# Kernel tuning notes

Measured on AMD Instinct MI355X. Metric: run time of the kernel, lower is better.

## Reference

```python
import jax, jax.numpy as jnp
import numpy as np

NX = 768
N_HEAD = 12
N_CTX = 2048
BATCH = 4
EPS = 1e-5
NEG = -1000000000.0


def _layernorm(x, g, b):
    # NOTE: faithful to source bug: returns g + normalized + b (additive, not scale)
    u = jnp.mean(x, axis=-1, keepdims=True)
    s = jnp.mean((x - u) ** 2, axis=-1, keepdims=True)
    return g + (x - u) / jnp.sqrt(s + EPS) + b


def setup_inputs() -> dict:
    key = jax.random.key(0)
    ks = jax.random.split(key, 8)
    std = 0.02
    x = jax.random.normal(ks[0], (BATCH, N_CTX, NX), dtype=jnp.float32)
    w_attn = jax.random.normal(ks[1], (NX, 3 * NX), dtype=jnp.float32) * std
    b_attn = jnp.zeros((3 * NX,), jnp.float32)
    w_proj = jax.random.normal(ks[2], (NX, NX), dtype=jnp.float32) * std
    b_proj = jnp.zeros((NX,), jnp.float32)
    ln1_g = jnp.ones((NX,), jnp.float32)
    ln1_b = jnp.zeros((NX,), jnp.float32)
    w_fc = jax.random.normal(ks[3], (NX, 4 * NX), dtype=jnp.float32) * std
    b_fc = jnp.zeros((4 * NX,), jnp.float32)
    w_fc2 = jax.random.normal(ks[4], (4 * NX, NX), dtype=jnp.float32) * std
    b_fc2 = jnp.zeros((NX,), jnp.float32)
    ln2_g = jnp.ones((NX,), jnp.float32)
    ln2_b = jnp.zeros((NX,), jnp.float32)
    return dict(x=x, w_attn=w_attn, b_attn=b_attn, w_proj=w_proj, b_proj=b_proj,
                ln1_g=ln1_g, ln1_b=ln1_b, w_fc=w_fc, b_fc=b_fc,
                w_fc2=w_fc2, b_fc2=b_fc2, ln2_g=ln2_g, ln2_b=ln2_b)


def reference(x, w_attn, b_attn, w_proj, b_proj, ln1_g, ln1_b,
              w_fc, b_fc, w_fc2, b_fc2, ln2_g, ln2_b):
    B, S, D = x.shape
    dh = D // N_HEAD
    # --- attention (scale=False: no 1/sqrt(d)) ---
    qkv = x @ w_attn + b_attn                      # [B,S,3D]
    q, k, v = jnp.split(qkv, 3, axis=-1)
    q = q.reshape(B, S, N_HEAD, dh).transpose(0, 2, 1, 3)   # [B,H,S,dh]
    k = k.reshape(B, S, N_HEAD, dh).transpose(0, 2, 3, 1)   # [B,H,dh,S]
    v = v.reshape(B, S, N_HEAD, dh).transpose(0, 2, 1, 3)   # [B,H,S,dh]
    w = jnp.einsum('bhsd,bhdt->bhst', q, k)        # [B,H,S,S]
    mask = jnp.tril(jnp.ones((S, S), x.dtype))[None, None]
    w = w * mask + NEG * (1.0 - mask)
    w = jax.nn.softmax(w, axis=-1)
    a = jnp.einsum('bhst,bhtd->bhsd', w, v)        # [B,H,S,dh]
    a = a.transpose(0, 2, 1, 3).reshape(B, S, D)
    a = a @ w_proj + b_proj
    # dropout layers are identity (eval mode)
    n = _layernorm(x + a, ln1_g, ln1_b)
    # --- MLP (intended ReLU; source's nn.ReLU usage is a bug) ---
    h = jax.nn.relu(n @ w_fc + b_fc)
    m = h @ w_fc2 + b_fc2
    return _layernorm(n + m, ln2_g, ln2_b)
```

## Files before the change

### kernel.cpp

```cpp
#include <hip/hip_runtime.h>
#include <stdint.h>

#define NX 768
#define SEQ 2048
#define NHEAD 12
#define MROWS 8192
#define LN_EPS 1e-5f
#define MASK_NEG -1000000000.0f

typedef __bf16 bf16x8 __attribute__((ext_vector_type(8)));
typedef float f32x4 __attribute__((ext_vector_type(4)));

#define AS3(p)  ((__attribute__((address_space(3))) void*)(p))
#define AS1C(p) ((const __attribute__((address_space(1))) void*)(p))

__device__ __forceinline__ unsigned short f2bf(float f) {
  union { float f; unsigned int u; } v; v.f = f;
  unsigned int r = v.u + 0x7fffu + ((v.u >> 16) & 1u);
  return (unsigned short)(r >> 16);
}
__device__ __forceinline__ unsigned int f2bf_fast_u(float f) {
  union { float f; unsigned int u; } v; v.f = f;
  return (v.u + 0x8000u) >> 16;
}
__device__ __forceinline__ float bf2f(unsigned short u) {
  union { unsigned int u; float f; } v; v.u = ((unsigned int)u) << 16;
  return v.f;
}

__global__ void convert_f32_bf16(const float* __restrict__ in,
                                 unsigned short* __restrict__ out, int n4) {
  int i = blockIdx.x * blockDim.x + threadIdx.x;
  if (i >= n4) return;
  float4 v = ((const float4*)in)[i];
  ushort4 o;
  o.x = f2bf(v.x); o.y = f2bf(v.y); o.z = f2bf(v.z); o.w = f2bf(v.w);
  ((ushort4*)out)[i] = o;
}

__global__ void transpose_w(const float* __restrict__ w,
                            unsigned short* __restrict__ wt, int K, int N) {
  __shared__ float tile[32][33];
  int n0 = blockIdx.x * 32, k0 = blockIdx.y * 32;
  int tx = threadIdx.x, ty = threadIdx.y;
#pragma unroll
  for (int j = 0; j < 4; ++j)
    tile[ty + j * 8][tx] = w[(long)(k0 + ty + j * 8) * N + n0 + tx];
  __syncthreads();
#pragma unroll
  for (int j = 0; j < 4; ++j)
    wt[(long)(n0 + ty + j * 8) * K + k0 + tx] = f2bf(tile[tx][ty + j * 8]);
}

__global__ void transpose_v(const unsigned short* __restrict__ qkv,
                            unsigned short* __restrict__ vt) {
  __shared__ unsigned short tile[64][68];
  int s0 = blockIdx.x * 64;
  int bh = blockIdx.y, b = bh / NHEAD, h = bh % NHEAD;
  int tx = threadIdx.x, ty = threadIdx.y;
  const unsigned short* src = qkv + (long)b * SEQ * 2304 + 1536 + h * 64;
#pragma unroll
  for (int j = 0; j < 4; ++j) {
    int s = ty + j * 16;
    ushort4 vv = *(const ushort4*)(src + (long)(s0 + s) * 2304 + tx * 4);
    *(ushort4*)(&tile[s][tx * 4]) = vv;
  }
  __syncthreads();
  unsigned short* dst = vt + (long)bh * 64 * SEQ + s0;
#pragma unroll
  for (int j = 0; j < 4; ++j) {
    int d = ty + j * 16;
    ushort4 o;
    o.x = tile[tx * 4 + 0][d]; o.y = tile[tx * 4 + 1][d];
    o.z = tile[tx * 4 + 2][d]; o.w = tile[tx * 4 + 3][d];
    *(ushort4*)(dst + (long)d * SEQ + tx * 4) = o;
  }
}

template <int ACT, int BN>
__global__ __launch_bounds__(256) void gemm_bt(const unsigned short* __restrict__ A,
                                               const unsigned short* __restrict__ Bt,
                                               const float* __restrict__ bias,
                                               unsigned short* __restrict__ C,
                                               int Nsz, int K) {
  constexpr int ABUF = 128 * 64;
  constexpr int BBUF = BN * 64;
  constexpr int BUF = ABUF + BBUF;
  __shared__ __align__(16) unsigned short smem[2 * BUF];
  const int tid = threadIdx.x;
  const int w = tid >> 6, lane = tid & 63;
  const int l15 = lane & 15, quad = lane >> 4;
  constexpr int MT = (BN == 128) ? 4 : 2;
  const int wrow0 = (BN == 128) ? (w >> 1) * 64 : w * 32;
  const int wcol0 = (BN == 128) ? (w & 1) * 64 : 0;
  const long m0 = (long)blockIdx.x * 128;
  const long n0 = (long)blockIdx.y * BN;

  const int srow = tid >> 3;
  const int sg = tid & 7;

  const unsigned short* ap[4];
#pragma unroll
  for (int p = 0; p < 4; ++p) {
    int row = p * 32 + srow;
    ap[p] = A + (m0 + row) * (long)K + (sg ^ (row & 7)) * 8;
  }
  const unsigned short* bp[BN / 32];
#pragma unroll
  for (int p = 0; p < BN / 32; ++p) {
    int row = p * 32 + srow;
    bp[p] = Bt + (n0 + row) * (long)K + (sg ^ (row & 7)) * 8;
  }

  auto stage = [&](int kb) {
    unsigned short* As = smem + (kb & 1) * BUF;
    unsigned short* Bs = As + ABUF;
#pragma unroll
    for (int p = 0; p < 4; ++p) {
      __builtin_amdgcn_global_load_lds(AS1C(ap[p]), AS3(As + p * 2048 + w * 512), 16, 0, 0);
      ap[p] += 64;
    }
#pragma unroll
    for (int p = 0; p < BN / 32; ++p) {
      __builtin_amdgcn_global_load_lds(AS1C(bp[p]), AS3(Bs + p * 2048 + w * 512), 16, 0, 0);
      bp[p] += 64;
    }
  };

  f32x4 acc[MT][4] = {};
  const int nkb = K / 64;

  stage(0);
  for (int kb = 0; kb < nkb; ++kb) {
    __syncthreads();
    if (kb + 1 < nkb) stage(kb + 1);
    const unsigned short* As = smem + (kb & 1) * BUF;
    const unsigned short* Bs = As + ABUF;
#pragma unroll
    for (int s2 = 0; s2 < 2; ++s2) {
      const int phys = ((s2 * 4 + quad) ^ (l15 & 7)) * 8;
      bf16x8 af[MT], bfr[4];
#pragma unroll
      for (int mt = 0; mt < MT; ++mt)
        af[mt] = *(const bf16x8*)(As + (wrow0 + mt * 16 + l15) * 64 + phys);
#pragma unroll
      for (int nt = 0; nt < 4; ++nt)
        bfr[nt] = *(const bf16x8*)(Bs + (wcol0 + nt * 16 + l15) * 64 + phys);
#pragma unroll
      for (int mt = 0; mt < MT; ++mt)
#pragma unroll
        for (int nt = 0; nt < 4; ++nt)
          acc[mt][nt] = __builtin_amdgcn_mfma_f32_16x16x32_bf16(af[mt], bfr[nt], acc[mt][nt], 0, 0, 0);
    }
  }
  __syncthreads();

  unsigned short* Ew = smem + w * (16 * 72);
  const long gmB = m0 + wrow0;
  const long gnB = n0 + wcol0;
  float bv[4];
#pragma unroll
  for (int nt = 0; nt < 4; ++nt) bv[nt] = bias[gnB + nt * 16 + l15];
  const int prow = lane >> 3, pcol = (lane & 7) * 8;
#pragma unroll
  for (int mt = 0; mt < MT; ++mt) {
#pragma unroll
    for (int nt = 0; nt < 4; ++nt)
#pragma unroll
      for (int r = 0; r < 4; ++r) {
        float v = acc[mt][nt][r] + bv[nt];
        if (ACT == 1) v = fmaxf(v, 0.f);
        Ew[(quad * 4 + r) * 72 + nt * 16 + l15] = f2bf(v);
      }
#pragma unroll
    for (int ps = 0; ps < 2; ++ps) {
      int row = ps * 8 + prow;
      int4 t = *(const int4*)(Ew + row * 72 + pcol);
      *(int4*)(C + (gmB + mt * 16 + row) * (long)Nsz + gnB + pcol) = t;
    }
  }
}

__global__ __launch_bounds__(256) void attn_v7(const unsigned short* __restrict__ qkv,
                                               const unsigned short* __restrict__ vt,
                                               unsigned short* __restrict__ out) {
  const int blk = blockIdx.x;
  const int bh_lo = blk & 7;
  const int j = blk >> 3;
  const int bx = j & 15;
  const int bh = (j >> 4) * 8 + bh_lo;
  const int b = bh / NHEAD, h = bh % NHEAD;
  const int tid = threadIdx.x;
  const int w = tid >> 6, lane = tid & 63, l15 = lane & 15, quad = lane >> 4;

  __shared__ __align__(16) unsigned short Ks[2][64 * 64];
  __shared__ __align__(16) unsigned short Vs[2][64 * 64];
  __shared__ __align__(16) unsigned short Ps[4][16 * 64];

  const long rowbase = (long)b * SEQ;
  unsigned short* Pw = &Ps[w][0];
  const unsigned short* vbh = vt + (long)bh * 64 * SEQ;
  const float LOG2E = 1.4426950408889634f;

  const int krow = tid >> 3;
  const int kgo = (((tid & 7) ^ (krow & 7)) * 8);
  const unsigned short* kbase = qkv + rowbase * 2304L + 768 + h * 64;

  for (int pass = 0; pass < 2; ++pass) {
    const int qt = (pass == 0) ? bx : 31 - bx;
    const int niter = qt + 1;
    const int qrow = qt * 64 + w * 16 + l15;
    const int qg = qrow;

    bf16x8 qf[2];
#pragma unroll
    for (int s2 = 0; s2 < 2; ++s2) {
      int4 raw = *(const int4*)(qkv + (rowbase + qrow) * 2304L + h * 64 + s2 * 32 + quad * 8);
      const unsigned short* rp = (const unsigned short*)&raw;
#pragma unroll
      for (int j2 = 0; j2 < 8; ++j2)
        qf[s2][j2] = (__bf16)(bf2f(rp[j2]) * LOG2E);
    }

    const unsigned short* kp[2];
    const unsigned short* vp[2];
#pragma unroll
    for (int p = 0; p < 2; ++p) {
      kp[p] = kbase + (long)(p * 32 + krow) * 2304 + kgo;
      vp[p] = vbh + (long)(p * 32 + krow) * SEQ + kgo;
    }

    float l_sum = 0.f;
    f32x4 o_acc[4] = {};

    __syncthreads();
#pragma unroll
    for (int p = 0; p < 2; ++p) {
      __builtin_amdgcn_global_load_lds(AS1C(kp[p]), AS3(&Ks[0][0] + p * 2048 + w * 512), 16, 0, 0);
      __builtin_amdgcn_global_load_lds(AS1C(vp[p]), AS3(&Vs[0][0] + p * 2048 + w * 512), 16, 0, 0);
      kp[p] += 64 * 2304;
      vp[p] += 64;
    }

    for (int it = 0; it < niter; ++it) {
      __syncthreads();
      if (it + 1 < niter) {
        const int nb = (it + 1) & 1;
#pragma unroll
        for (int p = 0; p < 2; ++p) {
          __builtin_amdgcn_global_load_lds(AS1C(kp[p]), AS3(&Ks[nb][0] + p * 2048 + w * 512), 16, 0, 0);
          __builtin_amdgcn_global_load_lds(AS1C(vp[p]), AS3(&Vs[nb][0] + p * 2048 + w * 512), 16, 0, 0);
          kp[p] += 64 * 2304;
          vp[p] += 64;
        }
      }
      const unsigned short* Kc = &Ks[it & 1][0];
      const unsigned short* Vc = &Vs[it & 1][0];

      f32x4 st[4] = {};
#pragma unroll
      for (int nt = 0; nt < 4; ++nt) {
        int key = nt * 16 + l15;
#pragma unroll
        for (int s2 = 0; s2 < 2; ++s2) {
          int phys = (s2 * 4 + quad) ^ (key & 7);
          bf16x8 kf = *(const bf16x8*)(Kc + key * 64 + phys * 8);
          st[nt] = __builtin_amdgcn_mfma_f32_16x16x32_bf16(kf, qf[s2], st[nt], 0, 0, 0);
        }
      }

      if (it == niter - 1) {
#pragma unroll
        for (int nt = 0; nt < 4; ++nt) {
          int kg = it * 64 + nt * 16 + quad * 4;
#pragma unroll
          for (int r = 0; r < 4; ++r)
            if (kg + r > qg) st[nt][r] = MASK_NEG;
        }
      }

      float psum = 0.f;
#pragma unroll
      for (int nt = 0; nt < 4; ++nt)
#pragma unroll
        for (int r = 0; r < 4; ++r) {
          float p = __builtin_amdgcn_exp2f(st[nt][r]);
          st[nt][r] = p;
          psum += p;
        }
      psum += __shfl_xor(psum, 16);
      psum += __shfl_xor(psum, 32);
      l_sum += psum;

#pragma unroll
      for (int nt = 0; nt < 4; ++nt) {
        unsigned int lo = f2bf_fast_u(st[nt][0]) | (f2bf_fast_u(st[nt][1]) << 16);
        unsigned int hi = f2bf_fast_u(st[nt][2]) | (f2bf_fast_u(st[nt][3]) << 16);
        int g8 = (nt * 2 + (quad >> 1)) ^ (l15 & 7);
        uint2 pv; pv.x = lo; pv.y = hi;
        *(uint2*)(Pw + l15 * 64 + g8 * 8 + (quad & 1) * 4) = pv;
      }

#pragma unroll
      for (int c = 0; c < 2; ++c) {
        int phys = ((c * 4 + quad) ^ (l15 & 7)) * 8;
        bf16x8 pf = *(const bf16x8*)(Pw + l15 * 64 + phys);
#pragma unroll
        for (int ntd = 0; ntd < 4; ++ntd) {
          int d = ntd * 16 + l15;
          bf16x8 vf = *(const bf16x8*)(Vc + d * 64 + phys);
          o_acc[ntd] = __builtin_amdgcn_mfma_f32_16x16x32_bf16(pf, vf, o_acc[ntd], 0, 0, 0);
        }
      }
    }

#pragma unroll
    for (int r = 0; r < 4; ++r) {
      float lq = __shfl(l_sum, quad * 4 + r);
      float inv = 1.f / lq;
      int q = qt * 64 + w * 16 + quad * 4 + r;
#pragma unroll
      for (int ntd = 0; ntd < 4; ++ntd) {
        int d = ntd * 16 + l15;
        out[(rowbase + q) * (long)NX + h * 64 + d] = f2bf(o_acc[ntd][r] * inv);
      }
    }
  }
}

__global__ __launch_bounds__(256) void add_ln(const float* __restrict__ x_f,
                                              const unsigned short* __restrict__ x_b,
                                              const unsigned short* __restrict__ y_b,
                                              const float* __restrict__ g,
                                              const float* __restrict__ beta,
                                              float* __restrict__ out_f,
                                              unsigned short* __restrict__ out_b) {
  const int row = blockIdx.x, t = threadIdx.x;
  const long base = (long)row * NX;
  float v[3];
#pragma unroll
  for (int j = 0; j < 3; ++j) {
    int i = t + j * 256;
    float a = x_f ? x_f[base + i] : bf2f(x_b[base + i]);
    v[j] = a + bf2f(y_b[base + i]);
  }
  __shared__ float red[4];
  int wv = t >> 6, ln = t & 63;

  float ssum = v[0] + v[1] + v[2];
#pragma unroll
  for (int sh = 32; sh >= 1; sh >>= 1) ssum += __shfl_xor(ssum, sh);
  if (ln == 0) red[wv] = ssum;
  __syncthreads();
  float u = (red[0] + red[1] + red[2] + red[3]) * (1.f / NX);
  __syncthreads();

  float d0 = v[0] - u, d1 = v[1] - u, d2 = v[2] - u;
  float sq = d0 * d0 + d1 * d1 + d2 * d2;
#pragma unroll
  for (int sh = 32; sh >= 1; sh >>= 1) sq += __shfl_xor(sq, sh);
  if (ln == 0) red[wv] = sq;
  __syncthreads();
  float s = (red[0] + red[1] + red[2] + red[3]) * (1.f / NX);
  float rinv = rsqrtf(s + LN_EPS);

  float dd[3] = {d0, d1, d2};
#pragma unroll
  for (int j = 0; j < 3; ++j) {
    int i = t + j * 256;
    float o = g[i] + dd[j] * rinv + beta[i];
    if (out_f) out_f[base + i] = o;
    else out_b[base + i] = f2bf(o);
  }
}

extern "C" void kernel_launch(void* const* d_in, const int* in_sizes, int n_in,
                              void* d_out, int out_size, void* d_ws, size_t ws_size,
                              hipStream_t stream) {
  const float* x      = (const float*)d_in[0];
  const float* w_attn = (const float*)d_in[1];
  const float* b_attn = (const float*)d_in[2];
  const float* w_proj = (const float*)d_in[3];
  const float* b_proj = (const float*)d_in[4];
  const float* ln1_g  = (const float*)d_in[5];
  const float* ln1_b  = (const float*)d_in[6];
  const float* w_fc   = (const float*)d_in[7];
  const float* b_fc   = (const float*)d_in[8];
  const float* w_fc2  = (const float*)d_in[9];
  const float* b_fc2  = (const float*)d_in[10];
  const float* ln2_g  = (const float*)d_in[11];
  const float* ln2_b  = (const float*)d_in[12];
  float* out = (float*)d_out;

  char* ws = (char*)d_ws;
  size_t off = 0;
  auto alloc = [&](size_t bytes) {
    char* p = ws + off;
    off += (bytes + 255) & ~(size_t)255;
    return p;
  };
  unsigned short* xb      = (unsigned short*)alloc((size_t)MROWS * NX * 2);
  unsigned short* wt_attn = (unsigned short*)alloc((size_t)2304 * 768 * 2);
  unsigned short* wt_proj = (unsigned short*)alloc((size_t)768 * 768 * 2);
  unsigned short* wt_fc   = (unsigned short*)alloc((size_t)3072 * 768 * 2);
  unsigned short* wt_fc2  = (unsigned short*)alloc((size_t)768 * 3072 * 2);
  unsigned short* qkv     = (unsigned short*)alloc((size_t)MROWS * 3072 * 2);
  unsigned short* hbuf    = qkv;
  unsigned short* abuf    = (unsigned short*)alloc((size_t)MROWS * NX * 2);
  unsigned short* mbuf    = abuf;
  unsigned short* nbuf    = (unsigned short*)alloc((size_t)MROWS * NX * 2);
  unsigned short* vtb     = nbuf;
  unsigned short* pout    = xb;

  convert_f32_bf16<<<(MROWS * NX / 4 + 255) / 256, 256, 0, stream>>>(x, xb, MROWS * NX / 4);
  transpose_w<<<dim3(2304 / 32, 768 / 32), dim3(32, 8), 0, stream>>>(w_attn, wt_attn, 768, 2304);
  transpose_w<<<dim3(768 / 32, 768 / 32), dim3(32, 8), 0, stream>>>(w_proj, wt_proj, 768, 768);
  transpose_w<<<dim3(3072 / 32, 768 / 32), dim3(32, 8), 0, stream>>>(w_fc, wt_fc, 768, 3072);
  transpose_w<<<dim3(768 / 32, 3072 / 32), dim3(32, 8), 0, stream>>>(w_fc2, wt_fc2, 3072, 768);

  gemm_bt<0, 64><<<dim3(MROWS / 128, 2304 / 64), 256, 0, stream>>>(xb, wt_attn, b_attn, qkv, 2304, 768);
  transpose_v<<<dim3(SEQ / 64, 48), dim3(16, 16), 0, stream>>>(qkv, vtb);
  attn_v7<<<768, 256, 0, stream>>>(qkv, vtb, abuf);
  gemm_bt<0, 64><<<dim3(MROWS / 128, 768 / 64), 256, 0, stream>>>(abuf, wt_proj, b_proj, pout, 768, 768);
  add_ln<<<MROWS, 256, 0, stream>>>(x, nullptr, pout, ln1_g, ln1_b, nullptr, nbuf);
  gemm_bt<1, 128><<<dim3(MROWS / 128, 3072 / 128), 256, 0, stream>>>(nbuf, wt_fc, b_fc, hbuf, 3072, 768);
  gemm_bt<0, 64><<<dim3(MROWS / 128, 768 / 64), 256, 0, stream>>>(hbuf, wt_fc2, b_fc2, mbuf, 768, 3072);
  add_ln<<<MROWS, 256, 0, stream>>>(nullptr, nbuf, mbuf, ln2_g, ln2_b, out, nullptr);
}
```

Measured before the change: 343.8 us.

## Split attention into one query tile per block, heaviest first, with hardware bf16 pack

The attention kernel previously handled two paired query tiles per block for causal load balance. Now each block handles a single query tile, launched longest-first (qt = 31 - t), which doubles the grid to 1536 blocks. The cross-lane row-sum shuffles are moved out of the key loop to run once at the end, and the bf16 packing of probabilities uses the v_cvt_pk_bf16_f32 instruction instead of manual integer rounding. The aim is better occupancy and tail scheduling plus less per-iteration ALU work, at the risk of blocks with very uneven work and a small rounding difference from the packed conversion.

```diff
diff --git a/kernel.cpp b/kernel.cpp
--- a/kernel.cpp
+++ b/kernel.cpp
@@ -18,10 +18,6 @@
   union { float f; unsigned int u; } v; v.f = f;
   unsigned int r = v.u + 0x7fffu + ((v.u >> 16) & 1u);
   return (unsigned short)(r >> 16);
-}
-__device__ __forceinline__ unsigned int f2bf_fast_u(float f) {
-  union { float f; unsigned int u; } v; v.f = f;
-  return (v.u + 0x8000u) >> 16;
 }
 __device__ __forceinline__ float bf2f(unsigned short u) {
   union { unsigned int u; float f; } v; v.u = ((unsigned int)u) << 16;
@@ -181,14 +177,15 @@
   }
 }
 
-__global__ __launch_bounds__(256) void attn_v7(const unsigned short* __restrict__ qkv,
+__global__ __launch_bounds__(256) void attn_v8(const unsigned short* __restrict__ qkv,
                                                const unsigned short* __restrict__ vt,
                                                unsigned short* __restrict__ out) {
   const int blk = blockIdx.x;
   const int bh_lo = blk & 7;
   const int j = blk >> 3;
-  const int bx = j & 15;
-  const int bh = (j >> 4) * 8 + bh_lo;
+  const int t = j & 31;
+  const int qt = 31 - t;
+  const int bh = (j >> 5) * 8 + bh_lo;
   const int b = bh / NHEAD, h = bh % NHEAD;
   const int tid = threadIdx.x;
   const int w = tid >> 6, lane = tid & 63, l15 = lane & 15, quad = lane >> 4;
@@ -206,124 +203,122 @@
   const int kgo = (((tid & 7) ^ (krow & 7)) * 8);
   const unsigned short* kbase = qkv + rowbase * 2304L + 768 + h * 64;
 
-  for (int pass = 0; pass < 2; ++pass) {
-    const int qt = (pass == 0) ? bx : 31 - bx;
-    const int niter = qt + 1;
-    const int qrow = qt * 64 + w * 16 + l15;
-    const int qg = qrow;
-
-    bf16x8 qf[2];
-#pragma unroll
-    for (int s2 = 0; s2 < 2; ++s2) {
-      int4 raw = *(const int4*)(qkv + (rowbase + qrow) * 2304L + h * 64 + s2 * 32 + quad * 8);
-      const unsigned short* rp = (const unsigned short*)&raw;
-#pragma unroll
-      for (int j2 = 0; j2 < 8; ++j2)
-        qf[s2][j2] = (__bf16)(bf2f(rp[j2]) * LOG2E);
-    }
-
-    const unsigned short* kp[2];
-    const unsigned short* vp[2];
-#pragma unroll
-    for (int p = 0; p < 2; ++p) {
-      kp[p] = kbase + (long)(p * 32 + krow) * 2304 + kgo;
-      vp[p] = vbh + (long)(p * 32 + krow) * SEQ + kgo;
-    }
-
-    float l_sum = 0.f;
-    f32x4 o_acc[4] = {};
-
+  const int niter = qt + 1;
+  const int qrow = qt * 64 + w * 16 + l15;
+  const int qg = qrow;
+
+  bf16x8 qf[2];
+#pragma unroll
+  for (int s2 = 0; s2 < 2; ++s2) {
+    int4 raw = *(const int4*)(qkv + (rowbase + qrow) * 2304L + h * 64 + s2 * 32 + quad * 8);
+    const unsigned short* rp = (const unsigned short*)&raw;
+#pragma unroll
+    for (int j2 = 0; j2 < 8; ++j2)
+      qf[s2][j2] = (__bf16)(bf2f(rp[j2]) * LOG2E);
+  }
+
+  const unsigned short* kp[2];
+  const unsigned short* vp[2];
+#pragma unroll
+  for (int p = 0; p < 2; ++p) {
+    kp[p] = kbase + (long)(p * 32 + krow) * 2304 + kgo;
+    vp[p] = vbh + (long)(p * 32 + krow) * SEQ + kgo;
+  }
+
+  float l_sum = 0.f;
+  f32x4 o_acc[4] = {};
+
+#pragma unroll
+  for (int p = 0; p < 2; ++p) {
+    __builtin_amdgcn_global_load_lds(AS1C(kp[p]), AS3(&Ks[0][0] + p * 2048 + w * 512), 16, 0, 0);
+    __builtin_amdgcn_global_load_lds(AS1C(vp[p]), AS3(&Vs[0][0] + p * 2048 + w * 512), 16, 0, 0);
+    kp[p] += 64 * 2304;
+    vp[p] += 64;
+  }
+
+  for (int it = 0; it < niter; ++it) {
     __syncthreads();
-#pragma unroll
-    for (int p = 0; p < 2; ++p) {
-      __builtin_amdgcn_global_load_lds(AS1C(kp[p]), AS3(&Ks[0][0] + p * 2048 + w * 512), 16, 0, 0);
-      __builtin_amdgcn_global_load_lds(AS1C(vp[p]), AS3(&Vs[0][0] + p * 2048 + w * 512), 16, 0, 0);
-      kp[p] += 64 * 2304;
-      vp[p] += 64;
-    }
-
-    for (int it = 0; it < niter; ++it) {
-      __syncthreads();
-      if (it + 1 < niter) {
-        const int nb = (it + 1) & 1;
-#pragma unroll
-        for (int p = 0; p < 2; ++p) {
-          __builtin_amdgcn_global_load_lds(AS1C(kp[p]), AS3(&Ks[nb][0] + p * 2048 + w * 512), 16, 0, 0);
-          __builtin_amdgcn_global_load_lds(AS1C(vp[p]), AS3(&Vs[nb][0] + p * 2048 + w * 512), 16, 0, 0);
-          kp[p] += 64 * 2304;
-          vp[p] += 64;
-        }
+    if (it + 1 < niter) {
+      const int nb = (it + 1) & 1;
+#pragma unroll
+      for (int p = 0; p < 2; ++p) {
+        __builtin_amdgcn_global_load_lds(AS1C(kp[p]), AS3(&Ks[nb][0] + p * 2048 + w * 512), 16, 0, 0);
+        __builtin_amdgcn_global_load_lds(AS1C(vp[p]), AS3(&Vs[nb][0] + p * 2048 + w * 512), 16, 0, 0);
+        kp[p] += 64 * 2304;
+        vp[p] += 64;
       }
-      const unsigned short* Kc = &Ks[it & 1][0];
-      const unsigned short* Vc = &Vs[it & 1][0];
-
-      f32x4 st[4] = {};
+    }
+    const unsigned short* Kc = &Ks[it & 1][0];
+    const unsigned short* Vc = &Vs[it & 1][0];
+
+    f32x4 st[4] = {};
+#pragma unroll
+    for (int nt = 0; nt < 4; ++nt) {
+      int key = nt * 16 + l15;
+#pragma unroll
+      for (int s2 = 0; s2 < 2; ++s2) {
+        int phys = (s2 * 4 + quad) ^ (key & 7);
+        bf16x8 kf = *(const bf16x8*)(Kc + key * 64 + phys * 8);
+        st[nt] = __builtin_amdgcn_mfma_f32_16x16x32_bf16(kf, qf[s2], st[nt], 0, 0, 0);
+      }
+    }
+
+    if (it == niter - 1) {
 #pragma unroll
       for (int nt = 0; nt < 4; ++nt) {
-        int key = nt * 16 + l15;
-#pragma unroll
-        for (int s2 = 0; s2 < 2; ++s2) {
-          int phys = (s2 * 4 + quad) ^ (key & 7);
-          bf16x8 kf = *(const bf16x8*)(Kc + key * 64 + phys * 8);
-          st[nt] = __builtin_amdgcn_mfma_f32_16x16x32_bf16(kf, qf[s2], st[nt], 0, 0, 0);
-        }
+        int kg = it * 64 + nt * 16 + quad * 4;
+#pragma unroll
+        for (int r = 0; r < 4; ++r)
+          if (kg + r > qg) st[nt][r] = MASK_NEG;
       }
-
-      if (it == niter - 1) {
-#pragma unroll
-        for (int nt = 0; nt < 4; ++nt) {
-          int kg = it * 64 + nt * 16 + quad * 4;
-#pragma unroll
-          for (int r = 0; r < 4; ++r)
-            if (kg + r > qg) st[nt][r] = MASK_NEG;
-        }
-      }
-
-      float psum = 0.f;
-#pragma unroll
-      for (int nt = 0; nt < 4; ++nt)
-#pragma unroll
-        for (int r = 0; r < 4; ++r) {
-          float p = __builtin_amdgcn_exp2f(st[nt][r]);
-          st[nt][r] = p;
-          psum += p;
-        }
-      psum += __shfl_xor(psum, 16);
-      psum += __shfl_xor(psum, 32);
-      l_sum += psum;
-
-#pragma unroll
-      for (int nt = 0; nt < 4; ++nt) {
-        unsigned int lo = f2bf_fast_u(st[nt][0]) | (f2bf_fast_u(st[nt][1]) << 16);
-        unsigned int hi = f2bf_fast_u(st[nt][2]) | (f2bf_fast_u(st[nt][3]) << 16);
-        int g8 = (nt * 2 + (quad >> 1)) ^ (l15 & 7);
-        uint2 pv; pv.x = lo; pv.y = hi;
-        *(uint2*)(Pw + l15 * 64 + g8 * 8 + (quad & 1) * 4) = pv;
-      }
-
-#pragma unroll
-      for (int c = 0; c < 2; ++c) {
-        int phys = ((c * 4 + quad) ^ (l15 & 7)) * 8;
-        bf16x8 pf = *(const bf16x8*)(Pw + l15 * 64 + phys);
-#pragma unroll
-        for (int ntd = 0; ntd < 4; ++ntd) {
-          int d = ntd * 16 + l15;
-          bf16x8 vf = *(const bf16x8*)(Vc + d * 64 + phys);
-          o_acc[ntd] = __builtin_amdgcn_mfma_f32_16x16x32_bf16(pf, vf, o_acc[ntd], 0, 0, 0);
-        }
-      }
-    }
-
-#pragma unroll
-    for (int r = 0; r < 4; ++r) {
-      float lq = __shfl(l_sum, quad * 4 + r);
-      float inv = 1.f / lq;
-      int q = qt * 64 + w * 16 + quad * 4 + r;
+    }
+
+    float sn[4];
+#pragma unroll
+    for (int nt = 0; nt < 4; ++nt) {
+      float p0 = __builtin_amdgcn_exp2f(st[nt][0]);
+      float p1 = __builtin_amdgcn_exp2f(st[nt][1]);
+      float p2 = __builtin_amdgcn_exp2f(st[nt][2]);
+      float p3 = __builtin_amdgcn_exp2f(st[nt][3]);
+      st[nt][0] = p0; st[nt][1] = p1; st[nt][2] = p2; st[nt][3] = p3;
+      sn[nt] = (p0 + p1) + (p2 + p3);
+    }
+    l_sum += (sn[0] + sn[1]) + (sn[2] + sn[3]);
+
+#pragma unroll
+    for (int nt = 0; nt < 4; ++nt) {
+      unsigned int lo, hi;
+      asm("v_cvt_pk_bf16_f32 %0, %1, %2" : "=v"(lo) : "v"(st[nt][0]), "v"(st[nt][1]));
+      asm("v_cvt_pk_bf16_f32 %0, %1, %2" : "=v"(hi) : "v"(st[nt][2]), "v"(st[nt][3]));
+      int g8 = (nt * 2 + (quad >> 1)) ^ (l15 & 7);
+      uint2 pv; pv.x = lo; pv.y = hi;
+      *(uint2*)(Pw + l15 * 64 + g8 * 8 + (quad & 1) * 4) = pv;
+    }
+
+#pragma unroll
+    for (int c = 0; c < 2; ++c) {
+      int phys = ((c * 4 + quad) ^ (l15 & 7)) * 8;
+      bf16x8 pf = *(const bf16x8*)(Pw + l15 * 64 + phys);
 #pragma unroll
       for (int ntd = 0; ntd < 4; ++ntd) {
         int d = ntd * 16 + l15;
-        out[(rowbase + q) * (long)NX + h * 64 + d] = f2bf(o_acc[ntd][r] * inv);
+        bf16x8 vf = *(const bf16x8*)(Vc + d * 64 + phys);
+        o_acc[ntd] = __builtin_amdgcn_mfma_f32_16x16x32_bf16(pf, vf, o_acc[ntd], 0, 0, 0);
       }
+    }
+  }
+
+  l_sum += __shfl_xor(l_sum, 16);
+  l_sum += __shfl_xor(l_sum, 32);
+#pragma unroll
+  for (int r = 0; r < 4; ++r) {
+    float lq = __shfl(l_sum, quad * 4 + r);
+    float inv = 1.f / lq;
+    int q = qt * 64 + w * 16 + quad * 4 + r;
+#pragma unroll
+    for (int ntd = 0; ntd < 4; ++ntd) {
+      int d = ntd * 16 + l15;
+      out[(rowbase + q) * (long)NX + h * 64 + d] = f2bf(o_acc[ntd][r] * inv);
     }
   }
 }
@@ -420,7 +415,7 @@
 
   gemm_bt<0, 64><<<dim3(MROWS / 128, 2304 / 64), 256, 0, stream>>>(xb, wt_attn, b_attn, qkv, 2304, 768);
   transpose_v<<<dim3(SEQ / 64, 48), dim3(16, 16), 0, stream>>>(qkv, vtb);
-  attn_v7<<<768, 256, 0, stream>>>(qkv, vtb, abuf);
+  attn_v8<<<1536, 256, 0, stream>>>(qkv, vtb, abuf);
   gemm_bt<0, 64><<<dim3(MROWS / 128, 768 / 64), 256, 0, stream>>>(abuf, wt_proj, b_proj, pout, 768, 768);
   add_ln<<<MROWS, 256, 0, stream>>>(x, nullptr, pout, ln1_g, ln1_b, nullptr, nbuf);
   gemm_bt<1, 128><<<dim3(MROWS / 128, 3072 / 128), 256, 0, stream>>>(nbuf, wt_fc, b_fc, hbuf, 3072, 768);
```

After: 348.5 us. Within noise of the previous version (+1.4%).
